# Kernel tuning notes

Measured on AMD Instinct MI355X. Metric: run time of the kernel, lower is better.

Reference implementation:

```python
import jax, jax.numpy as jnp
import numpy as np

# ---- model hyperparameters (match init_kwargs) ----
D_MODEL = 1024
D_STATE = 128
EXPAND = 2
HEADDIM = 64
NGROUPS = 1
D_INNER = EXPAND * D_MODEL            # 2048
NHEADS = D_INNER // HEADDIM           # 32
ROPE_FRAC = 0.5
SPLIT = int(D_STATE * ROPE_FRAC)      # 64 rotary dims
NANG = SPLIT // 2                     # 32 rope angles
A_FLOOR = 1e-4
EPS = 1e-5
BATCH, SEQLEN = 1, 1024
SIZES = [D_INNER, D_INNER, D_STATE * NGROUPS, D_STATE * NGROUPS, NHEADS, NHEADS, NHEADS, NANG]
D_IN_PROJ = int(np.sum(SIZES))        # 4480


def setup_inputs() -> dict:
    key = jax.random.key(0)
    ks = jax.random.split(key, 6)
    u = jax.random.normal(ks[0], (BATCH, SEQLEN, D_MODEL), dtype=jnp.float32)
    W_in = jax.random.normal(ks[1], (D_MODEL, D_IN_PROJ), dtype=jnp.float32) * 0.02
    # dt_bias ~ log(dt) for dt in [1e-3, 0.1] -> around -4
    dt_bias = jax.random.normal(ks[2], (NHEADS,), dtype=jnp.float32) * 0.5 - 4.0
    B_bias = jnp.ones((NHEADS, D_STATE), jnp.float32) + 0.01 * jax.random.normal(ks[3], (NHEADS, D_STATE), dtype=jnp.float32)
    C_bias = jnp.ones((NHEADS, D_STATE), jnp.float32) + 0.01 * jax.random.normal(ks[4], (NHEADS, D_STATE), dtype=jnp.float32)
    Bn_w = jnp.ones((D_STATE,), jnp.float32)
    Cn_w = jnp.ones((D_STATE,), jnp.float32)
    D_param = jnp.ones((NHEADS,), jnp.float32)
    W_out = jax.random.normal(ks[5], (D_INNER, D_MODEL), dtype=jnp.float32) * 0.02
    return {"u": u, "W_in": W_in, "dt_bias": dt_bias, "B_bias": B_bias, "C_bias": C_bias,
            "Bn_w": Bn_w, "Cn_w": Cn_w, "D_param": D_param, "W_out": W_out}


def _rmsnorm(v, w):
    return v * jax.lax.rsqrt(jnp.mean(v * v, axis=-1, keepdims=True) + EPS) * w


def _forward(u, W_in, dt_bias, B_bias, C_bias, Bn_w, Cn_w, D_param, W_out):
    b, l, _ = u.shape
    proj = u @ W_in                                   # (b, l, d_in_proj)
    idx = np.cumsum(SIZES)[:-1]
    z, x, Bp, Cp, dd_dt, dd_A, trap_raw, ang = jnp.split(proj, idx, axis=-1)
    z = z.reshape(b, l, NHEADS, HEADDIM)
    x = x.reshape(b, l, NHEADS, HEADDIM)
    # A = clamp(-softplus(.), max=-A_floor);  dt = softplus(. + dt_bias)
    A = jnp.minimum(-jax.nn.softplus(dd_A), -A_FLOOR)          # (b,l,H)
    dt = jax.nn.softplus(dd_dt + dt_bias)                      # (b,l,H)
    a = jnp.exp(A * dt)                                        # decay per step
    lam = jax.nn.sigmoid(trap_raw)                             # trapezoid gate
    # RMSNorm on B/C (ngroups=1), then per-head additive bias
    Bn = _rmsnorm(Bp, Bn_w)                                    # (b,l,N)
    Cn = _rmsnorm(Cp, Cn_w)
    Bh = Bn[:, :, None, :] + B_bias                            # (b,l,H,N)
    Ch = Cn[:, :, None, :] + C_bias
    # data-dependent rotary: cumulative angle = cumsum(angles * dt)
    theta = jnp.cumsum(ang[:, :, None, :] * dt[..., None], axis=1)  # (b,l,H,NANG)
    cos, sin = jnp.cos(theta), jnp.sin(theta)

    def rope(v):
        d1, d2, rest = v[..., :NANG], v[..., NANG:SPLIT], v[..., SPLIT:]
        return jnp.concatenate([d1 * cos - d2 * sin, d1 * sin + d2 * cos, rest], axis=-1)

    Bh, Ch = rope(Bh), rope(Ch)

    tfirst = lambda v: jnp.moveaxis(v, 1, 0)
    inputs = (tfirst(Bh), tfirst(Ch), tfirst(x), tfirst(a), tfirst(dt), tfirst(lam))
    h0 = jnp.zeros((b, NHEADS, HEADDIM, D_STATE), jnp.float32)
    k0 = jnp.zeros((b, NHEADS, D_STATE), jnp.float32)
    v0 = jnp.zeros((b, NHEADS, HEADDIM), jnp.float32)

    def step(carry, inp):
        h, kp, vp = carry
        Bt, Ct, xt, at, dtt, lamt = inp
        # trapezoidal selective-scan update:
        # h_t = a_t h_{t-1} + dt_t (lam_t B_t x_t + (1-lam_t) a_t B_{t-1} x_{t-1})
        cur = jnp.einsum('bhp,bhn->bhpn', xt, Bt) * (dtt * lamt)[..., None, None]
        prv = jnp.einsum('bhp,bhn->bhpn', vp, kp) * (dtt * (1.0 - lamt) * at)[..., None, None]
        h = at[..., None, None] * h + cur + prv
        yt = jnp.einsum('bhn,bhpn->bhp', Ct, h)
        return (h, Bt, xt), yt

    _, y = jax.lax.scan(step, (h0, k0, v0), inputs)          # (l,b,H,P)
    y = jnp.moveaxis(y, 0, 1) + D_param[None, None, :, None] * x
    y = y * jax.nn.silu(z)                                    # gated output (no out-proj norm)
    return y.reshape(b, l, D_INNER) @ W_out


def reference(u, W_in, dt_bias, B_bias, C_bias, Bn_w, Cn_w, D_param, W_out):
    return _forward(u, W_in, dt_bias, B_bias, C_bias, Bn_w, Cn_w, D_param, W_out)
```

## Files before the change

### kernel.cpp

```cpp
#include <hip/hip_runtime.h>
#include <stdint.h>

#define SEQ     1024

typedef __attribute__((ext_vector_type(8))) short short8;
typedef __attribute__((ext_vector_type(4))) float f4;

__device__ __forceinline__ short f2b(float f){
  union { float f; uint32_t u; } v; v.f = f;
  uint32_t r = (v.u + 0x7fffu + ((v.u >> 16) & 1u)) >> 16;
  return (short)(uint16_t)r;
}
__device__ __forceinline__ float b2f(uint16_t u){
  union { uint32_t u; float f; } v; v.u = ((uint32_t)u) << 16; return v.f;
}
__device__ __forceinline__ uint32_t pack2(float lo, float hi){
  return (uint32_t)(uint16_t)f2b(lo) | ((uint32_t)(uint16_t)f2b(hi) << 16);
}
__device__ __forceinline__ float softplus_f(float x){
  return x > 20.f ? x : log1pf(__expf(x));
}
__device__ __forceinline__ void gload_lds16(const short* g, short* l){
  __builtin_amdgcn_global_load_lds((const __attribute__((address_space(1))) void*)g,
                                   (__attribute__((address_space(3))) void*)l, 16, 0, 0);
}

__global__ __launch_bounds__(256) void prep_inputs(const float* __restrict__ u, short* __restrict__ u16,
                                                   const float* __restrict__ W_in, short* __restrict__ WtIn,
                                                   const float* __restrict__ W_out, short* __restrict__ WtOut,
                                                   float* __restrict__ outz){
  int b = blockIdx.x;
  int tid = threadIdx.x;
  if (b < 1024){
    int i = (b * 256 + tid) * 4;
    f4 v = *(const f4*)(u + i);
    uint2 pk; pk.x = pack2(v.x, v.y); pk.y = pack2(v.z, v.w);
    *(uint2*)(u16 + i) = pk;
    return;
  }
  if (b >= 2656){
    int i = ((b - 2656) * 256 + tid) * 4;
    *(f4*)(outz + i) = (f4){0.f, 0.f, 0.f, 0.f};
    return;
  }
  const float* in; short* outp; int R, lda, bx, by;
  if (b < 2144){ int idx = b - 1024; bx = idx % 140; by = idx / 140; in = W_in;  outp = WtIn;  R = 1024; lda = 4480; }
  else         { int idx = b - 2144; bx = idx & 31;  by = idx >> 5;  in = W_out; outp = WtOut; R = 2048; lda = 1024; }
  __shared__ float tile[32][132];
  int bc = bx * 32, br = by * 128;
  int c = tid & 31, r0 = tid >> 5;
  #pragma unroll
  for (int i = 0; i < 16; i++){
    int r = r0 + i * 8;
    tile[c][r] = in[(size_t)(br + r) * lda + bc + c];
  }
  __syncthreads();
  #pragma unroll
  for (int i = 0; i < 4; i++){
    int task = tid + 256 * i;
    int cc = task >> 5;
    int rg = (task & 31) * 4;
    f4 v = *(const f4*)&tile[cc][rg];
    uint2 pk; pk.x = pack2(v.x, v.y); pk.y = pack2(v.z, v.w);
    *(uint2*)(outp + (size_t)(bc + cc) * R + br + rg) = pk;
  }
}

__global__ __launch_bounds__(256) void gemm1_kernel(const short* __restrict__ A, const short* __restrict__ Bt,
                                                    short* __restrict__ zx, short* __restrict__ xTb,
                                                    float* __restrict__ projT){
  const int K = 1024;
  __shared__ __align__(16) short As[2][128 * 64];
  __shared__ __align__(16) short Bs[2][160 * 64];
  const int tid  = threadIdx.x;
  const int wave = tid >> 6;
  const int lane = tid & 63;
  const int m0 = blockIdx.y * 128;
  const int n0 = blockIdx.x * 160;
  const int wm = (wave >> 1) * 64;
  const int wn = (wave & 1) * 80;
  const int quad = lane >> 4;
  const int r16  = lane & 15;
  const int rsw  = r16 & 7;

  f4 acc[4][5];
  #pragma unroll
  for (int i = 0; i < 4; i++)
    #pragma unroll
    for (int j = 0; j < 5; j++) acc[i][j] = (f4){0.f, 0.f, 0.f, 0.f};

  const int srow = tid >> 3;
  const int soct = tid & 7;
  const int og   = (soct ^ (srow & 7)) * 8;
  const short* gA0 = A  + (size_t)(m0 + srow) * K + og;
  const short* gB0 = Bt + (size_t)(n0 + srow) * K + og;

  #pragma unroll
  for (int i = 0; i < 4; i++) gload_lds16(gA0 + (size_t)i * 32 * K, &As[0][tid * 8 + i * 2048]);
  #pragma unroll
  for (int i = 0; i < 5; i++) gload_lds16(gB0 + (size_t)i * 32 * K, &Bs[0][tid * 8 + i * 2048]);

  for (int kt = 0; kt < 16; ++kt){
    const int cur = kt & 1;
    __syncthreads();
    if (kt + 1 < 16){
      const int ko = (kt + 1) * 64;
      const int nxt = cur ^ 1;
      #pragma unroll
      for (int i = 0; i < 4; i++) gload_lds16(gA0 + (size_t)i * 32 * K + ko, &As[nxt][tid * 8 + i * 2048]);
      #pragma unroll
      for (int i = 0; i < 5; i++) gload_lds16(gB0 + (size_t)i * 32 * K + ko, &Bs[nxt][tid * 8 + i * 2048]);
    }
    #pragma unroll
    for (int ks = 0; ks < 2; ++ks){
      const int oq = ((ks * 4 + quad) ^ rsw) * 8;
      short8 af[4], bf[5];
      #pragma unroll
      for (int i = 0; i < 4; i++)
        af[i] = *(const short8*)&As[cur][(wm + i * 16 + r16) * 64 + oq];
      #pragma unroll
      for (int j = 0; j < 5; j++)
        bf[j] = *(const short8*)&Bs[cur][(wn + j * 16 + r16) * 64 + oq];
      #pragma unroll
      for (int i = 0; i < 4; i++)
        #pragma unroll
        for (int j = 0; j < 5; j++)
          acc[i][j] = __builtin_amdgcn_mfma_f32_16x16x32_bf16(af[i], bf[j], acc[i][j], 0, 0, 0);
    }
  }

  #pragma unroll
  for (int i = 0; i < 4; i++)
    #pragma unroll
    for (int j = 0; j < 5; j++){
      int colb = n0 + wn + j * 16 + r16;
      int rowb = m0 + wm + i * 16 + quad * 4;
      if (colb < 2048){
        #pragma unroll
        for (int rr = 0; rr < 4; ++rr)
          zx[(size_t)(rowb + rr) * 4096 + colb] = f2b(acc[i][j][rr]);
      } else if (colb < 4096){
        uint2 pk; pk.x = pack2(acc[i][j][0], acc[i][j][1]); pk.y = pack2(acc[i][j][2], acc[i][j][3]);
        *(uint2*)(xTb + (size_t)(colb - 2048) * 1024 + rowb) = pk;
        #pragma unroll
        for (int rr = 0; rr < 4; ++rr)
          zx[(size_t)(rowb + rr) * 4096 + colb] = f2b(acc[i][j][rr]);
      } else {
        #pragma unroll
        for (int rr = 0; rr < 4; ++rr)
          projT[(size_t)(rowb + rr) * 384 + (colb - 4096)] = acc[i][j][rr];
      }
    }
}

__global__ __launch_bounds__(256) void gemm2_kernel(const short* __restrict__ A, const short* __restrict__ Bt,
                                                    float* __restrict__ C){
  const int N = 1024, K = 2048, klen = 1024;
  __shared__ __align__(16) short As[2][64 * 64];
  __shared__ __align__(16) short Bs[2][128 * 64];
  const int tid  = threadIdx.x;
  const int wave = tid >> 6;
  const int lane = tid & 63;
  const int m0 = blockIdx.y * 64;
  const int n0 = blockIdx.x * 128;
  const int k0 = blockIdx.z * klen;
  const int wm = (wave >> 1) * 32;
  const int wn = (wave & 1) * 64;
  const int quad = lane >> 4;
  const int r16  = lane & 15;
  const int rsw  = r16 & 7;

  f4 acc[2][4];
  #pragma unroll
  for (int i = 0; i < 2; i++)
    #pragma unroll
    for (int j = 0; j < 4; j++) acc[i][j] = (f4){0.f, 0.f, 0.f, 0.f};

  const int srow = tid >> 3;
  const int soct = tid & 7;
  const int og   = (soct ^ (srow & 7)) * 8;
  const short* gA0 = A  + (size_t)(m0 + srow) * K + k0 + og;
  const short* gB0 = Bt + (size_t)(n0 + srow) * K + k0 + og;

  #pragma unroll
  for (int i = 0; i < 2; i++) gload_lds16(gA0 + (size_t)i * 32 * K, &As[0][tid * 8 + i * 2048]);
  #pragma unroll
  for (int i = 0; i < 4; i++) gload_lds16(gB0 + (size_t)i * 32 * K, &Bs[0][tid * 8 + i * 2048]);

  for (int kt = 0; kt < 16; ++kt){
    const int cur = kt & 1;
    __syncthreads();
    if (kt + 1 < 16){
      const int ko = (kt + 1) * 64;
      const int nxt = cur ^ 1;
      #pragma unroll
      for (int i = 0; i < 2; i++) gload_lds16(gA0 + (size_t)i * 32 * K + ko, &As[nxt][tid * 8 + i * 2048]);
      #pragma unroll
      for (int i = 0; i < 4; i++) gload_lds16(gB0 + (size_t)i * 32 * K + ko, &Bs[nxt][tid * 8 + i * 2048]);
    }
    #pragma unroll
    for (int ks = 0; ks < 2; ++ks){
      const int oq = ((ks * 4 + quad) ^ rsw) * 8;
      short8 af[2], bf[4];
      #pragma unroll
      for (int i = 0; i < 2; i++)
        af[i] = *(const short8*)&As[cur][(wm + i * 16 + r16) * 64 + oq];
      #pragma unroll
      for (int j = 0; j < 4; j++)
        bf[j] = *(const short8*)&Bs[cur][(wn + j * 16 + r16) * 64 + oq];
      #pragma unroll
      for (int i = 0; i < 2; i++)
        #pragma unroll
        for (int j = 0; j < 4; j++)
          acc[i][j] = __builtin_amdgcn_mfma_f32_16x16x32_bf16(af[i], bf[j], acc[i][j], 0, 0, 0);
    }
  }

  #pragma unroll
  for (int i = 0; i < 2; i++)
    #pragma unroll
    for (int j = 0; j < 4; j++)
      #pragma unroll
      for (int rr = 0; rr < 4; ++rr){
        int row = m0 + wm + i * 16 + quad * 4 + rr;
        int col = n0 + wn + j * 16 + r16;
        unsafeAtomicAdd(&C[(size_t)row * N + col], acc[i][j][rr]);
      }
}

__global__ __launch_bounds__(256) void scan_theta(const float* __restrict__ projT,
                                                  const float* __restrict__ dt_bias,
                                                  float* __restrict__ Lcum, float* __restrict__ u2b,
                                                  float* __restrict__ c1b,
                                                  float* __restrict__ cosb, float* __restrict__ sinb){
  int b = blockIdx.x;
  int tid = threadIdx.x;
  int t0 = tid * 4;
  int lane = tid & 63, wave = tid >> 6;
  __shared__ float wsum[4];
  if (b < 32){
    int h = b;
    float dtbias = dt_bias[h];
    float dt5[5], lam5[5];
    #pragma unroll
    for (int i = 0; i < 5; i++){
      int t = t0 + i;
      if (t < 1024){
        const float* row = projT + (size_t)t * 384;
        dt5[i]  = softplus_f(row[256 + h] + dtbias);
        lam5[i] = 1.f / (1.f + __expf(-row[320 + h]));
      } else { dt5[i] = 0.f; lam5[i] = 0.f; }
    }
    float v[4], c1[4], c2n[4];
    #pragma unroll
    for (int i = 0; i < 4; i++){
      int t = t0 + i;
      const float* row = projT + (size_t)t * 384;
      float Ah = -fmaxf(softplus_f(row[288 + h]), 1e-4f);
      v[i]   = Ah * dt5[i];
      c1[i]  = dt5[i] * lam5[i];
      c2n[i] = dt5[i + 1] * (1.f - lam5[i + 1]);
    }
    v[1] += v[0]; v[2] += v[1]; v[3] += v[2];
    float tot = v[3], sc = tot;
    #pragma unroll
    for (int off = 1; off < 64; off <<= 1){
      float n = __shfl_up(sc, off, 64);
      if (lane >= off) sc += n;
    }
    if (lane == 63) wsum[wave] = sc;
    __syncthreads();
    float base = sc - tot;
    for (int w = 0; w < wave; ++w) base += wsum[w];
    #pragma unroll
    for (int i = 0; i < 4; i++){
      int t = t0 + i;
      Lcum[h * 1024 + t] = base + v[i];
      u2b[h * 1024 + t]  = c1[i] + c2n[i];
      c1b[h * 1024 + t]  = c1[i];
    }
  } else {
    int hk = b - 32;
    int h = hk >> 5, k = hk & 31;
    float dtbias = dt_bias[h];
    float v[4];
    #pragma unroll
    for (int i = 0; i < 4; i++){
      const float* row = projT + (size_t)(t0 + i) * 384;
      float dt = softplus_f(row[256 + h] + dtbias);
      v[i] = row[352 + k] * dt;
    }
    v[1] += v[0]; v[2] += v[1]; v[3] += v[2];
    float tot = v[3], sc = tot;
    #pragma unroll
    for (int off = 1; off < 64; off <<= 1){
      float n = __shfl_up(sc, off, 64);
      if (lane >= off) sc += n;
    }
    if (lane == 63) wsum[wave] = sc;
    __syncthreads();
    float base = sc - tot;
    for (int w = 0; w < wave; ++w) base += wsum[w];
    #pragma unroll
    for (int i = 0; i < 4; i++){
      float th = base + v[i];
      float s, c;
      __sincosf(th, &s, &c);
      int t = t0 + i;
      cosb[(size_t)t * 1024 + h * 32 + k] = c;
      sinb[(size_t)t * 1024 + h * 32 + k] = s;
    }
  }
}

__global__ __launch_bounds__(256) void bcxt_kernel(const float* __restrict__ projT,
                                                   const float* __restrict__ B_bias, const float* __restrict__ C_bias,
                                                   const float* __restrict__ Bn_w, const float* __restrict__ Cn_w,
                                                   const float* __restrict__ cosb, const float* __restrict__ sinb,
                                                   short* __restrict__ Bb, short* __restrict__ Cb){
  int t = blockIdx.x;
  int tid = threadIdx.x;
  __shared__ float vv[2][128];
  __shared__ float red[4];
  int n = tid & 127;
  int isC = tid >> 7;
  float val = projT[(size_t)t * 384 + isC * 128 + n];
  float ss = val * val;
  #pragma unroll
  for (int off = 32; off >= 1; off >>= 1) ss += __shfl_down(ss, off);
  int wave = tid >> 6, lane = tid & 63;
  if (lane == 0) red[wave] = ss;
  __syncthreads();
  float rsv = isC ? rsqrtf((red[2] + red[3]) * (1.f / 128.f) + 1e-5f)
                  : rsqrtf((red[0] + red[1]) * (1.f / 128.f) + 1e-5f);
  vv[isC][n] = val * rsv * (isC ? Cn_w[n] : Bn_w[n]);
  __syncthreads();
  const float* cb = cosb + (size_t)t * 1024;
  const float* sb = sinb + (size_t)t * 1024;
  #pragma unroll
  for (int it = 0; it < 8; it++){
    int task = tid + 256 * it;
    int arr  = task >> 10;
    int rem  = task & 1023;
    int h    = rem >> 5;
    int n0   = (rem & 31) * 4;
    const float* bias = arr ? C_bias : B_bias;
    const float* base = vv[arr];
    f4 bv = *(const f4*)&base[n0];
    f4 bi = *(const f4*)&bias[h * 128 + n0];
    f4 o;
    if (n0 < 32){
      f4 bv2 = *(const f4*)&base[n0 + 32];
      f4 bi2 = *(const f4*)&bias[h * 128 + n0 + 32];
      f4 cv = *(const f4*)&cb[h * 32 + n0];
      f4 sv = *(const f4*)&sb[h * 32 + n0];
      #pragma unroll
      for (int q = 0; q < 4; q++) o[q] = (bv[q] + bi[q]) * cv[q] - (bv2[q] + bi2[q]) * sv[q];
    } else if (n0 < 64){
      int k0 = n0 - 32;
      f4 bv1 = *(const f4*)&base[k0];
      f4 bi1 = *(const f4*)&bias[h * 128 + k0];
      f4 cv = *(const f4*)&cb[h * 32 + k0];
      f4 sv = *(const f4*)&sb[h * 32 + k0];
      #pragma unroll
      for (int q = 0; q < 4; q++) o[q] = (bv1[q] + bi1[q]) * sv[q] + (bv[q] + bi[q]) * cv[q];
    } else {
      #pragma unroll
      for (int q = 0; q < 4; q++) o[q] = bv[q] + bi[q];
    }
    uint2 pk; pk.x = pack2(o.x, o.y); pk.y = pack2(o.z, o.w);
    short* outp = arr ? Cb : Bb;
    *(uint2*)(outp + (size_t)t * 4096 + h * 128 + n0) = pk;
  }
}

__global__ __launch_bounds__(256) void hpart_kernel(const short* __restrict__ xTb, const short* __restrict__ Bb,
                                                    const float* __restrict__ Lcum, const float* __restrict__ u2b,
                                                    short* __restrict__ Hpart){
  int h = blockIdx.x >> 4, c = (blockIdx.x >> 1) & 7, nh = blockIdx.x & 1;
  int t0 = c * 128;
  int tid = threadIdx.x;
  __shared__ float wS[128];
  if (tid < 128){
    float Lend = Lcum[h * 1024 + t0 + 127];
    wS[tid] = __expf(Lend - Lcum[h * 1024 + t0 + tid]) * u2b[h * 1024 + t0 + tid];
  }
  __syncthreads();
  int wave = tid >> 6, lane = tid & 63, quad = lane >> 4, r16 = lane & 15;
  int n0 = nh * 64 + wave * 16;
  f4 acc[4];
  #pragma unroll
  for (int i = 0; i < 4; i++) acc[i] = (f4){0.f, 0.f, 0.f, 0.f};

  const ushort* Bh = (const ushort*)Bb + (size_t)t0 * 4096 + h * 128;
  #pragma unroll
  for (int kk = 0; kk < 4; ++kk){
    int sb = kk * 32 + quad * 8;
    short8 af[4];
    #pragma unroll
    for (int i = 0; i < 4; i++){
      int p = i * 16 + r16;
      af[i] = *(const short8*)(xTb + (size_t)(h * 64 + p) * 1024 + t0 + sb);
    }
    float wv[8];
    #pragma unroll
    for (int jj = 0; jj < 8; jj++) wv[jj] = wS[sb + jj];
    int nn = n0 + r16;
    float e[8];
    #pragma unroll
    for (int jj = 0; jj < 8; jj++)
      e[jj] = b2f(Bh[(size_t)(sb + jj) * 4096 + nn]) * wv[jj];
    union { short8 s; uint32_t u[4]; } fr;
    #pragma unroll
    for (int q = 0; q < 4; q++) fr.u[q] = pack2(e[2 * q], e[2 * q + 1]);
    short8 bfr = fr.s;
    #pragma unroll
    for (int i = 0; i < 4; i++)
      acc[i] = __builtin_amdgcn_mfma_f32_16x16x32_bf16(af[i], bfr, acc[i], 0, 0, 0);
  }

  short* out = Hpart + ((size_t)(h * 8 + c)) * 8192;
  int nn = n0 + r16;
  #pragma unroll
  for (int i = 0; i < 4; i++)
    #pragma unroll
    for (int rr = 0; rr < 4; ++rr){
      int p = i * 16 + quad * 4 + rr;
      out[p * 128 + nn] = f2b(acc[i][rr]);
    }
}

#define GS 144
__global__ __launch_bounds__(256) void chunky_kernel(const short* __restrict__ Cb, const short* __restrict__ Bbg,
                                                     const short* __restrict__ xTb, const short* __restrict__ Hpart,
                                                     const float* __restrict__ Lcum, const float* __restrict__ u2b,
                                                     const float* __restrict__ c1b,
                                                     const short* __restrict__ zx, const float* __restrict__ D_par,
                                                     short* __restrict__ yb16){
  int h = blockIdx.x >> 4, c = (blockIdx.x >> 1) & 7, half = blockIdx.x & 1;
  int t0 = c * 128;
  int tb = half * 64;
  __shared__ __align__(16) short Gt[64 * GS];
  __shared__ __align__(16) short Hu[64 * 128];
  __shared__ float Lc[128], u2v[128], c1v[128];
  int tid = threadIdx.x;
  if (tid < 128){
    Lc[tid]  = Lcum[h * 1024 + t0 + tid];
    u2v[tid] = u2b[h * 1024 + t0 + tid];
    c1v[tid] = c1b[h * 1024 + t0 + tid];
  }
  float Lprev = (c > 0) ? Lcum[h * 1024 + t0 - 1] : 0.f;
  float Dp = D_par[h];

  {
    float hacc[32];
    #pragma unroll
    for (int q = 0; q < 32; q++) hacc[q] = 0.f;
    for (int cp = 0; cp < c; ++cp){
      float dec = __expf(Lprev - Lcum[h * 1024 + cp * 128 + 127]);
      const short8* hp = (const short8*)((const ushort*)Hpart + ((size_t)(h * 8 + cp)) * 8192 + tid * 32);
      #pragma unroll
      for (int q = 0; q < 4; q++){
        short8 v = hp[q];
        #pragma unroll
        for (int e = 0; e < 8; e++) hacc[q * 8 + e] += dec * b2f((uint16_t)v[e]);
      }
    }
    int p = tid >> 2;
    int wbase = tid * 64;
    #pragma unroll
    for (int q = 0; q < 4; q++){
      union { short8 s; uint32_t u[4]; } fr;
      #pragma unroll
      for (int p2 = 0; p2 < 4; p2++) fr.u[p2] = pack2(hacc[q * 8 + p2 * 2], hacc[q * 8 + p2 * 2 + 1]);
      int off = (wbase + q * 16) ^ ((p & 7) << 4);
      *(short8*)((char*)Hu + off) = fr.s;
    }
  }

  int wave = tid >> 6, lane = tid & 63, quad = lane >> 4, r16 = lane & 15;
  int wm2 = (wave >> 1) * 32, wn2 = (wave & 1) * 64;

  f4 acc[2][4];
  #pragma unroll
  for (int i = 0; i < 2; i++)
    #pragma unroll
    for (int j = 0; j < 4; j++) acc[i][j] = (f4){0.f, 0.f, 0.f, 0.f};
  #pragma unroll
  for (int kk = 0; kk < 4; ++kk){
    short8 af[2], bf[4];
    #pragma unroll
    for (int i = 0; i < 2; i++)
      af[i] = *(const short8*)(Cb + (size_t)(t0 + tb + wm2 + i * 16 + r16) * 4096 + h * 128 + kk * 32 + quad * 8);
    #pragma unroll
    for (int j = 0; j < 4; j++)
      bf[j] = *(const short8*)(Bbg + (size_t)(t0 + wn2 + j * 16 + r16) * 4096 + h * 128 + kk * 32 + quad * 8);
    #pragma unroll
    for (int i = 0; i < 2; i++)
      #pragma unroll
      for (int j = 0; j < 4; j++)
        acc[i][j] = __builtin_amdgcn_mfma_f32_16x16x32_bf16(af[i], bf[j], acc[i][j], 0, 0, 0);
  }
  __syncthreads();

  #pragma unroll
  for (int i = 0; i < 2; i++){
    #pragma unroll
    for (int rr = 0; rr < 4; ++rr){
      int tl = wm2 + i * 16 + quad * 4 + rr;
      int trow = tb + tl;
      float Lt = Lc[trow];
      #pragma unroll
      for (int j = 0; j < 4; j++){
        int scol = wn2 + j * 16 + r16;
        float g = 0.f;
        if (scol <= trow){
          float wcoef = (scol == trow) ? c1v[scol] : u2v[scol];
          g = acc[i][j][rr] * wcoef * __expf(Lt - Lc[scol]);
        }
        Gt[tl * GS + scol] = f2b(g);
      }
    }
  }
  __syncthreads();

  f4 accY[4], accZ[4];
  #pragma unroll
  for (int j = 0; j < 4; j++){ accY[j] = (f4){0.f,0.f,0.f,0.f}; accZ[j] = (f4){0.f,0.f,0.f,0.f}; }
  int m0 = wave * 16;
  #pragma unroll
  for (int kk = 0; kk < 4; ++kk){
    short8 ag, ac, bx[4], bh[4];
    ag = *(const short8*)&Gt[(m0 + r16) * GS + kk * 32 + quad * 8];
    ac = *(const short8*)(Cb + (size_t)(t0 + tb + m0 + r16) * 4096 + h * 128 + kk * 32 + quad * 8);
    #pragma unroll
    for (int j = 0; j < 4; j++){
      bx[j] = *(const short8*)(xTb + (size_t)(h * 64 + j * 16 + r16) * 1024 + t0 + kk * 32 + quad * 8);
      int hrow = j * 16 + r16;
      int hoff = (hrow * 256 + kk * 64 + quad * 16) ^ ((hrow & 7) << 4);
      bh[j] = *(const short8*)((const char*)Hu + hoff);
    }
    #pragma unroll
    for (int j = 0; j < 4; j++){
      accY[j] = __builtin_amdgcn_mfma_f32_16x16x32_bf16(ag, bx[j], accY[j], 0, 0, 0);
      accZ[j] = __builtin_amdgcn_mfma_f32_16x16x32_bf16(ac, bh[j], accZ[j], 0, 0, 0);
    }
  }
  const ushort* zxu = (const ushort*)zx;
  #pragma unroll
  for (int rr = 0; rr < 4; ++rr){
    int tl = m0 + quad * 4 + rr;
    int trow = tb + tl;
    float ei = __expf(Lc[trow] - Lprev);
    const ushort* zrow = zxu + (size_t)(t0 + trow) * 4096;
    #pragma unroll
    for (int j = 0; j < 4; j++){
      int col = h * 64 + j * 16 + r16;
      float zv = b2f(zrow[col]);
      float xv = b2f(zrow[2048 + col]);
      float yv = accY[j][rr] + ei * accZ[j][rr] + Dp * xv;
      float o = yv * (zv / (1.f + __expf(-zv)));
      yb16[(size_t)(t0 + trow) * 2048 + col] = f2b(o);
    }
  }
}

extern "C" void kernel_launch(void* const* d_in, const int* in_sizes, int n_in,
                              void* d_out, int out_size, void* d_ws, size_t ws_size,
                              hipStream_t stream){
  const float* u       = (const float*)d_in[0];
  const float* W_in    = (const float*)d_in[1];
  const float* dt_bias = (const float*)d_in[2];
  const float* B_bias  = (const float*)d_in[3];
  const float* C_bias  = (const float*)d_in[4];
  const float* Bn_w    = (const float*)d_in[5];
  const float* Cn_w    = (const float*)d_in[6];
  const float* D_par   = (const float*)d_in[7];
  const float* W_out   = (const float*)d_in[8];
  float* out = (float*)d_out;

  char* ws = (char*)d_ws;
  short* u16   = (short*)(ws + 0);
  short* WtIn  = (short*)(ws + 2097152);
  short* WtOut = (short*)(ws + 11272192);
  short* zx    = (short*)(ws + 15466496);
  float* projT = (float*)(ws + 23855104);
  float* cosb  = (float*)(ws + 25427968);
  float* sinb  = (float*)(ws + 29622272);
  short* Bb    = (short*)(ws + 33816576);
  short* Cb    = (short*)(ws + 42205184);
  short* xTb   = (short*)(ws + 50593792);
  float* Lcum  = (float*)(ws + 54788096);
  float* u2b   = (float*)(ws + 54919168);
  float* c1b   = (float*)(ws + 55050240);
  short* Hpart = (short*)(ws + 55181312);
  short* yb16  = (short*)(ws + 59375616);

  prep_inputs<<<3680, 256, 0, stream>>>(u, u16, W_in, WtIn, W_out, WtOut, out);
  gemm1_kernel<<<dim3(28, 8), 256, 0, stream>>>(u16, WtIn, zx, xTb, projT);
  scan_theta<<<1056, 256, 0, stream>>>(projT, dt_bias, Lcum, u2b, c1b, cosb, sinb);
  bcxt_kernel<<<1024, 256, 0, stream>>>(projT, B_bias, C_bias, Bn_w, Cn_w, cosb, sinb, Bb, Cb);
  hpart_kernel<<<512, 256, 0, stream>>>(xTb, Bb, Lcum, u2b, Hpart);
  chunky_kernel<<<512, 256, 0, stream>>>(Cb, Bb, xTb, Hpart, Lcum, u2b, c1b, zx, D_par, yb16);
  gemm2_kernel<<<dim3(8, 16, 2), 256, 0, stream>>>(yb16, WtOut, out);
}
```

Measured before the change: 211.4 us.

## Triple-buffer GEMM LDS pipelines, shrink gemm1 tiles, deepen gemm2 split-K

Both GEMMs move from a double-buffered LDS pipeline to a three-stage ring. Loads run two tiles ahead, and explicit vmcnt waits with raw barriers replace __syncthreads. gemm1 drops from 128x160 tiles to 64x128, giving 560 blocks instead of 224 so more CUs are covered. gemm2's split-K grows from 2 to 4, which raises block count but doubles the atomic adds into the output. The hand-placed waitcnt values depend on the exact number of outstanding loads per stage, so correctness hinges on that count being right.

```diff
diff --git a/kernel.cpp b/kernel.cpp
--- a/kernel.cpp
+++ b/kernel.cpp
@@ -70,24 +70,24 @@
                                                     short* __restrict__ zx, short* __restrict__ xTb,
                                                     float* __restrict__ projT){
   const int K = 1024;
-  __shared__ __align__(16) short As[2][128 * 64];
-  __shared__ __align__(16) short Bs[2][160 * 64];
+  __shared__ __align__(16) short As[3][64 * 64];
+  __shared__ __align__(16) short Bs[3][128 * 64];
   const int tid  = threadIdx.x;
   const int wave = tid >> 6;
   const int lane = tid & 63;
-  const int m0 = blockIdx.y * 128;
-  const int n0 = blockIdx.x * 160;
-  const int wm = (wave >> 1) * 64;
-  const int wn = (wave & 1) * 80;
+  const int m0 = blockIdx.y * 64;
+  const int n0 = blockIdx.x * 128;
+  const int wm = (wave >> 1) * 32;
+  const int wn = (wave & 1) * 64;
   const int quad = lane >> 4;
   const int r16  = lane & 15;
   const int rsw  = r16 & 7;
 
-  f4 acc[4][5];
-  #pragma unroll
-  for (int i = 0; i < 4; i++)
-    #pragma unroll
-    for (int j = 0; j < 5; j++) acc[i][j] = (f4){0.f, 0.f, 0.f, 0.f};
+  f4 acc[2][4];
+  #pragma unroll
+  for (int i = 0; i < 2; i++)
+    #pragma unroll
+    for (int j = 0; j < 4; j++) acc[i][j] = (f4){0.f, 0.f, 0.f, 0.f};
 
   const int srow = tid >> 3;
   const int soct = tid & 7;
@@ -95,44 +95,53 @@
   const short* gA0 = A  + (size_t)(m0 + srow) * K + og;
   const short* gB0 = Bt + (size_t)(n0 + srow) * K + og;
 
-  #pragma unroll
-  for (int i = 0; i < 4; i++) gload_lds16(gA0 + (size_t)i * 32 * K, &As[0][tid * 8 + i * 2048]);
-  #pragma unroll
-  for (int i = 0; i < 5; i++) gload_lds16(gB0 + (size_t)i * 32 * K, &Bs[0][tid * 8 + i * 2048]);
+#define G1_STAGE(buf, kt) do {                                              \
+    const int ko_ = (kt) * 64;                                              \
+    gload_lds16(gA0 + ko_,                   &As[buf][tid * 8]);            \
+    gload_lds16(gA0 + (size_t)32 * K + ko_,  &As[buf][tid * 8 + 2048]);     \
+    gload_lds16(gB0 + ko_,                   &Bs[buf][tid * 8]);            \
+    gload_lds16(gB0 + (size_t)32 * K + ko_,  &Bs[buf][tid * 8 + 2048]);     \
+    gload_lds16(gB0 + (size_t)64 * K + ko_,  &Bs[buf][tid * 8 + 4096]);     \
+    gload_lds16(gB0 + (size_t)96 * K + ko_,  &Bs[buf][tid * 8 + 6144]);     \
+  } while(0)
+
+  G1_STAGE(0, 0);
+  G1_STAGE(1, 1);
 
   for (int kt = 0; kt < 16; ++kt){
-    const int cur = kt & 1;
-    __syncthreads();
-    if (kt + 1 < 16){
-      const int ko = (kt + 1) * 64;
-      const int nxt = cur ^ 1;
-      #pragma unroll
-      for (int i = 0; i < 4; i++) gload_lds16(gA0 + (size_t)i * 32 * K + ko, &As[nxt][tid * 8 + i * 2048]);
-      #pragma unroll
-      for (int i = 0; i < 5; i++) gload_lds16(gB0 + (size_t)i * 32 * K + ko, &Bs[nxt][tid * 8 + i * 2048]);
-    }
+    if (kt < 15) asm volatile("s_waitcnt vmcnt(6)" ::: "memory");
+    else         asm volatile("s_waitcnt vmcnt(0)" ::: "memory");
+    __builtin_amdgcn_s_barrier();
+    __builtin_amdgcn_sched_barrier(0);
+    if (kt + 2 < 16){
+      int nb = kt + 2 - ((kt + 2) / 3) * 3;
+      G1_STAGE(nb, kt + 2);
+    }
+    const short* Ac = As[kt % 3];
+    const short* Bc = Bs[kt % 3];
     #pragma unroll
     for (int ks = 0; ks < 2; ++ks){
       const int oq = ((ks * 4 + quad) ^ rsw) * 8;
-      short8 af[4], bf[5];
-      #pragma unroll
-      for (int i = 0; i < 4; i++)
-        af[i] = *(const short8*)&As[cur][(wm + i * 16 + r16) * 64 + oq];
-      #pragma unroll
-      for (int j = 0; j < 5; j++)
-        bf[j] = *(const short8*)&Bs[cur][(wn + j * 16 + r16) * 64 + oq];
-      #pragma unroll
-      for (int i = 0; i < 4; i++)
+      short8 af[2], bf[4];
+      #pragma unroll
+      for (int i = 0; i < 2; i++)
+        af[i] = *(const short8*)&Ac[(wm + i * 16 + r16) * 64 + oq];
+      #pragma unroll
+      for (int j = 0; j < 4; j++)
+        bf[j] = *(const short8*)&Bc[(wn + j * 16 + r16) * 64 + oq];
+      #pragma unroll
+      for (int i = 0; i < 2; i++)
         #pragma unroll
-        for (int j = 0; j < 5; j++)
+        for (int j = 0; j < 4; j++)
           acc[i][j] = __builtin_amdgcn_mfma_f32_16x16x32_bf16(af[i], bf[j], acc[i][j], 0, 0, 0);
     }
   }
-
-  #pragma unroll
-  for (int i = 0; i < 4; i++)
-    #pragma unroll
-    for (int j = 0; j < 5; j++){
+#undef G1_STAGE
+
+  #pragma unroll
+  for (int i = 0; i < 2; i++)
+    #pragma unroll
+    for (int j = 0; j < 4; j++){
       int colb = n0 + wn + j * 16 + r16;
       int rowb = m0 + wm + i * 16 + quad * 4;
       if (colb < 2048){
@@ -155,15 +164,15 @@
 
 __global__ __launch_bounds__(256) void gemm2_kernel(const short* __restrict__ A, const short* __restrict__ Bt,
                                                     float* __restrict__ C){
-  const int N = 1024, K = 2048, klen = 1024;
-  __shared__ __align__(16) short As[2][64 * 64];
-  __shared__ __align__(16) short Bs[2][128 * 64];
+  const int N = 1024, K = 2048;
+  __shared__ __align__(16) short As[3][64 * 64];
+  __shared__ __align__(16) short Bs[3][128 * 64];
   const int tid  = threadIdx.x;
   const int wave = tid >> 6;
   const int lane = tid & 63;
   const int m0 = blockIdx.y * 64;
   const int n0 = blockIdx.x * 128;
-  const int k0 = blockIdx.z * klen;
+  const int k0 = blockIdx.z * 512;
   const int wm = (wave >> 1) * 32;
   const int wn = (wave & 1) * 64;
   const int quad = lane >> 4;
@@ -182,32 +191,40 @@
   const short* gA0 = A  + (size_t)(m0 + srow) * K + k0 + og;
   const short* gB0 = Bt + (size_t)(n0 + srow) * K + k0 + og;
 
-  #pragma unroll
-  for (int i = 0; i < 2; i++) gload_lds16(gA0 + (size_t)i * 32 * K, &As[0][tid * 8 + i * 2048]);
-  #pragma unroll
-  for (int i = 0; i < 4; i++) gload_lds16(gB0 + (size_t)i * 32 * K, &Bs[0][tid * 8 + i * 2048]);
-
-  for (int kt = 0; kt < 16; ++kt){
-    const int cur = kt & 1;
-    __syncthreads();
-    if (kt + 1 < 16){
-      const int ko = (kt + 1) * 64;
-      const int nxt = cur ^ 1;
-      #pragma unroll
-      for (int i = 0; i < 2; i++) gload_lds16(gA0 + (size_t)i * 32 * K + ko, &As[nxt][tid * 8 + i * 2048]);
-      #pragma unroll
-      for (int i = 0; i < 4; i++) gload_lds16(gB0 + (size_t)i * 32 * K + ko, &Bs[nxt][tid * 8 + i * 2048]);
-    }
+#define G2_STAGE(buf, kt) do {                                              \
+    const int ko_ = (kt) * 64;                                              \
+    gload_lds16(gA0 + ko_,                   &As[buf][tid * 8]);            \
+    gload_lds16(gA0 + (size_t)32 * K + ko_,  &As[buf][tid * 8 + 2048]);     \
+    gload_lds16(gB0 + ko_,                   &Bs[buf][tid * 8]);            \
+    gload_lds16(gB0 + (size_t)32 * K + ko_,  &Bs[buf][tid * 8 + 2048]);     \
+    gload_lds16(gB0 + (size_t)64 * K + ko_,  &Bs[buf][tid * 8 + 4096]);     \
+    gload_lds16(gB0 + (size_t)96 * K + ko_,  &Bs[buf][tid * 8 + 6144]);     \
+  } while(0)
+
+  G2_STAGE(0, 0);
+  G2_STAGE(1, 1);
+
+  for (int kt = 0; kt < 8; ++kt){
+    if (kt < 7) asm volatile("s_waitcnt vmcnt(6)" ::: "memory");
+    else        asm volatile("s_waitcnt vmcnt(0)" ::: "memory");
+    __builtin_amdgcn_s_barrier();
+    __builtin_amdgcn_sched_barrier(0);
+    if (kt + 2 < 8){
+      int nb = kt + 2 - ((kt + 2) / 3) * 3;
+      G2_STAGE(nb, kt + 2);
+    }
+    const short* Ac = As[kt % 3];
+    const short* Bc = Bs[kt % 3];
     #pragma unroll
     for (int ks = 0; ks < 2; ++ks){
       const int oq = ((ks * 4 + quad) ^ rsw) * 8;
       short8 af[2], bf[4];
       #pragma unroll
       for (int i = 0; i < 2; i++)
-        af[i] = *(const short8*)&As[cur][(wm + i * 16 + r16) * 64 + oq];
+        af[i] = *(const short8*)&Ac[(wm + i * 16 + r16) * 64 + oq];
       #pragma unroll
       for (int j = 0; j < 4; j++)
-        bf[j] = *(const short8*)&Bs[cur][(wn + j * 16 + r16) * 64 + oq];
+        bf[j] = *(const short8*)&Bc[(wn + j * 16 + r16) * 64 + oq];
       #pragma unroll
       for (int i = 0; i < 2; i++)
         #pragma unroll
@@ -215,6 +232,7 @@
           acc[i][j] = __builtin_amdgcn_mfma_f32_16x16x32_bf16(af[i], bf[j], acc[i][j], 0, 0, 0);
     }
   }
+#undef G2_STAGE
 
   #pragma unroll
   for (int i = 0; i < 2; i++)
@@ -597,10 +615,10 @@
   short* yb16  = (short*)(ws + 59375616);
 
   prep_inputs<<<3680, 256, 0, stream>>>(u, u16, W_in, WtIn, W_out, WtOut, out);
-  gemm1_kernel<<<dim3(28, 8), 256, 0, stream>>>(u16, WtIn, zx, xTb, projT);
+  gemm1_kernel<<<dim3(35, 16), 256, 0, stream>>>(u16, WtIn, zx, xTb, projT);
   scan_theta<<<1056, 256, 0, stream>>>(projT, dt_bias, Lcum, u2b, c1b, cosb, sinb);
   bcxt_kernel<<<1024, 256, 0, stream>>>(projT, B_bias, C_bias, Bn_w, Cn_w, cosb, sinb, Bb, Cb);
   hpart_kernel<<<512, 256, 0, stream>>>(xTb, Bb, Lcum, u2b, Hpart);
   chunky_kernel<<<512, 256, 0, stream>>>(Cb, Bb, xTb, Hpart, Lcum, u2b, c1b, zx, D_par, yb16);
-  gemm2_kernel<<<dim3(8, 16, 2), 256, 0, stream>>>(yb16, WtOut, out);
-}
+  gemm2_kernel<<<dim3(8, 16, 4), 256, 0, stream>>>(yb16, WtOut, out);
+}
```

Result: faster. 201.7 us (-4.6%).
